# Performance work log

Measured on AMD Instinct MI355X. Metric: run time of the kernel, lower is better.

The kernel has to match this reference:

```python
import jax, jax.numpy as jnp
import numpy as np

B, N, H, E, STEPS = 8, 1024, 128, 4, 3


def setup_inputs() -> dict:
    key = jax.random.key(0)
    ks = jax.random.split(key, 12)
    node_features = jax.random.normal(ks[0], (B, N, H), dtype=jnp.float32)
    edge_matrix = (jax.random.uniform(ks[1], (B, E, N, N)) < 0.01).astype(jnp.float32)
    s = 1.0 / np.sqrt(H)
    We = jax.random.uniform(ks[2], (E, H, H), minval=-s, maxval=s)  # per-edge-type Linear weights (out,in)
    W_ih = jax.random.uniform(ks[3], (3 * H, H), minval=-s, maxval=s)
    W_hh = jax.random.uniform(ks[4], (3 * H, H), minval=-s, maxval=s)
    b_ih = jax.random.uniform(ks[5], (3 * H,), minval=-s, maxval=s)
    b_hh = jax.random.uniform(ks[6], (3 * H,), minval=-s, maxval=s)
    s2 = 1.0 / np.sqrt(2 * H)
    W1 = jax.random.uniform(ks[7], (H, 2 * H), minval=-s2, maxval=s2)
    b1 = jax.random.uniform(ks[8], (H,), minval=-s2, maxval=s2)
    W2 = jax.random.uniform(ks[9], (H, H), minval=-s, maxval=s)
    b2 = jax.random.uniform(ks[10], (H,), minval=-s, maxval=s)
    return dict(node_features=node_features, edge_matrix=edge_matrix, We=We,
                W_ih=W_ih, W_hh=W_hh, b_ih=b_ih, b_hh=b_hh,
                W1=W1, b1=b1, W2=W2, b2=b2)


def _gru_cell(m, h, W_ih, W_hh, b_ih, b_hh):
    # PyTorch GRUCell: gates ordered (r, z, n)
    gi = m @ W_ih.T + b_ih  # (..., 3H)
    gh = h @ W_hh.T + b_hh
    i_r, i_z, i_n = jnp.split(gi, 3, axis=-1)
    h_r, h_z, h_n = jnp.split(gh, 3, axis=-1)
    r = jax.nn.sigmoid(i_r + h_r)
    z = jax.nn.sigmoid(i_z + h_z)
    n = jnp.tanh(i_n + r * h_n)
    return (1.0 - z) * n + z * h


def reference(node_features, edge_matrix, We, W_ih, W_hh, b_ih, b_hh, W1, b1, W2, b2):
    h = node_features  # (B,N,H)
    for _ in range(STEPS):
        # fused per-edge-type Linear: t[b,e,j,k] = sum_h h[b,j,h] * We[e,k,h]
        t = jnp.einsum('bjh,ekh->bejk', h, We)
        # aggregate messages: m[b,i,k] = sum_{e,j} adj[b,e,i,j] * t[b,e,j,k]
        m = jnp.einsum('beij,bejk->bik', edge_matrix, t)
        h = _gru_cell(m, h, W_ih, W_hh, b_ih, b_hh)
    cat = jnp.concatenate([node_features, h], axis=-1)  # (B,N,2H)
    y = jax.nn.relu(cat @ W1.T + b1)
    return y @ W2.T + b2
```

## Files before the change

### kernel.cpp

```cpp
#include <hip/hip_runtime.h>
#include <stdint.h>

typedef short short8 __attribute__((ext_vector_type(8)));
typedef float f32x4 __attribute__((ext_vector_type(4)));

__device__ inline float b2f(unsigned short u) {
    union { float f; uint32_t i; } v; v.i = ((uint32_t)u) << 16; return v.f;
}
__device__ inline unsigned short f2b(float f) {
    union { float f; uint32_t i; } v; v.f = f;
    uint32_t r = v.i + 0x7FFFu + ((v.i >> 16) & 1u);
    return (unsigned short)(r >> 16);
}

#define BB 8
#define NN 1024
#define HH 128
#define EE 4
#define MROWS (BB * NN)
#define NBR_CAP 96
#define CMAX 88
#define RPB 32


__global__ __launch_bounds__(256) void combo(
    const float* __restrict__ adj, unsigned short* __restrict__ cols,
    int* __restrict__ cnt,
    const float* __restrict__ nf, const float* __restrict__ We,
    const float* __restrict__ Wih, const float* __restrict__ Whh,
    const float* __restrict__ bih, const float* __restrict__ bhh,
    const float* __restrict__ W1, const float* __restrict__ W2,
    float* __restrict__ h, unsigned short* __restrict__ hb,
    unsigned short* __restrict__ nfb,
    unsigned short* __restrict__ wcf, unsigned short* __restrict__ wgf,
    unsigned short* __restrict__ w1f, unsigned short* __restrict__ w2f,
    float* __restrict__ bg)
{
    if (blockIdx.x < 8192) {
        int blk = blockIdx.x;
        int gb = blk & 7, q = blk >> 3;
        int row = gb * 4096 + q * 4 + (threadIdx.x >> 6);
        int l = threadIdx.x & 63;
        const float* ar = adj + (size_t)row * NN;
        unsigned short* cr = cols + (size_t)row * NBR_CAP;
        int c = 0;
        for (int it = 0; it < 4; ++it) {
            float4 v = *(const float4*)(ar + it * 256 + l * 4);
            const float* vp = &v.x;
            #pragma unroll
            for (int p = 0; p < 4; ++p) {
                float x = vp[p];
                unsigned long long m = __ballot(x != 0.f);
                if (x != 0.f) {
                    int idx = c + __popcll(m & ((1ull << l) - 1ull));
                    if (idx < CMAX) cr[idx] = (unsigned short)(it * 256 + l * 4 + p);
                }
                c += __popcll(m);
            }
        }
        int bb = row >> 12;
        int cs = c < CMAX ? c : CMAX;
        int pad = (8 - (cs & 7)) & 7;
        if (l < pad) cr[cs + l] = (unsigned short)((8 - bb) << 10);
        if (l == 0) cnt[row] = cs + pad;
        return;
    }
    int blk2 = blockIdx.x - 8192;
    int gb = blk2 & 7, q = blk2 >> 3;
    int tid = (gb * 512 + q) * 256 + threadIdx.x;
    {
        float v = nf[tid];
        h[tid] = v;
        unsigned short b = f2b(v);
        hb[tid] = b;
        nfb[tid] = b;
    }
    if (tid < 128) hb[(size_t)MROWS * 128 + tid] = 0;
    if (tid < 131072) {
        int j = tid & 7, l = (tid >> 3) & 63, f = (tid >> 9) & 31, s = tid >> 14;
        int col = f * 16 + (l & 15);
        int k   = s * 32 + ((l >> 4) << 3) + j;
        int kr = k & 127;
        float v;
        if (col < 256)      v = (k < 128) ? Wih[col * 128 + kr] : Whh[col * 128 + kr];
        else if (col < 384) v = (k < 128) ? Wih[col * 128 + kr] : 0.f;
        else                v = (k < 128) ? 0.f : Whh[(col - 128) * 128 + kr];
        wgf[tid] = f2b(v);
    }
    if (tid < 65536) {
        int j = tid & 7, l = (tid >> 3) & 63, f = (tid >> 9) & 7, s = tid >> 12;
        int col = f * 16 + (l & 15);
        int k   = s * 32 + ((l >> 4) << 3) + j;
        int e = k >> 7, hh2 = k & 127;
        wcf[tid] = f2b(We[(e << 14) + (col << 7) + hh2]);
    }
    if (tid < 32768) {
        int j = tid & 7, l = (tid >> 3) & 63, f = (tid >> 9) & 7, s = tid >> 12;
        int col = f * 16 + (l & 15);
        int k   = s * 32 + ((l >> 4) << 3) + j;
        w1f[tid] = f2b(W1[col * 256 + k]);
    }
    if (tid < 16384) {
        int j = tid & 7, l = (tid >> 3) & 63, f = (tid >> 9) & 7, s = tid >> 12;
        int col = f * 16 + (l & 15);
        int k   = s * 32 + ((l >> 4) << 3) + j;
        w2f[tid] = f2b(W2[col * 128 + k]);
    }
    if (tid < 512) {
        int sec = tid >> 7, k = tid & 127;
        float v;
        if (sec == 0)      v = bih[k] + bhh[k];
        else if (sec == 1) v = bih[128 + k] + bhh[128 + k];
        else if (sec == 2) v = bih[256 + k];
        else               v = bhh[256 + k];
        bg[tid] = v;
    }
}

__global__ __launch_bounds__(256) void aggregate(
    const unsigned short* __restrict__ hb, const unsigned short* __restrict__ cols,
    const int* __restrict__ cnt, unsigned short* __restrict__ ab)
{
    int blk = blockIdx.x;
    int b = blk & 7, i = blk >> 3;
    int e = threadIdx.x >> 6;
    int l2 = (threadIdx.x & 63) * 2;
    int row = ((b << 2) + e) * NN + i;
    int c = cnt[row];
    const unsigned short* cl = cols + (size_t)row * NBR_CAP;
    const unsigned short* hbase = hb + ((size_t)(b << 10)) * HH + l2;
    float a0 = 0.f, a1 = 0.f;
    for (int q = 0; q < c; q += 8) {
        uint4 iv = *(const uint4*)(cl + q);
        uint32_t v0 = *(const uint32_t*)(hbase + (size_t)(iv.x & 0xffffu) * HH);
        uint32_t v1 = *(const uint32_t*)(hbase + (size_t)(iv.x >> 16) * HH);
        uint32_t v2 = *(const uint32_t*)(hbase + (size_t)(iv.y & 0xffffu) * HH);
        uint32_t v3 = *(const uint32_t*)(hbase + (size_t)(iv.y >> 16) * HH);
        uint32_t v4 = *(const uint32_t*)(hbase + (size_t)(iv.z & 0xffffu) * HH);
        uint32_t v5 = *(const uint32_t*)(hbase + (size_t)(iv.z >> 16) * HH);
        uint32_t v6 = *(const uint32_t*)(hbase + (size_t)(iv.w & 0xffffu) * HH);
        uint32_t v7 = *(const uint32_t*)(hbase + (size_t)(iv.w >> 16) * HH);
        a0 += b2f((unsigned short)(v0 & 0xffffu)); a1 += b2f((unsigned short)(v0 >> 16));
        a0 += b2f((unsigned short)(v1 & 0xffffu)); a1 += b2f((unsigned short)(v1 >> 16));
        a0 += b2f((unsigned short)(v2 & 0xffffu)); a1 += b2f((unsigned short)(v2 >> 16));
        a0 += b2f((unsigned short)(v3 & 0xffffu)); a1 += b2f((unsigned short)(v3 >> 16));
        a0 += b2f((unsigned short)(v4 & 0xffffu)); a1 += b2f((unsigned short)(v4 >> 16));
        a0 += b2f((unsigned short)(v5 & 0xffffu)); a1 += b2f((unsigned short)(v5 >> 16));
        a0 += b2f((unsigned short)(v6 & 0xffffu)); a1 += b2f((unsigned short)(v6 >> 16));
        a0 += b2f((unsigned short)(v7 & 0xffffu)); a1 += b2f((unsigned short)(v7 >> 16));
    }
    *(uint32_t*)(ab + ((size_t)((b << 10) + i) * EE + e) * HH + l2) =
        (uint32_t)f2b(a0) | ((uint32_t)f2b(a1) << 16);
}

template<bool LAST>
__global__ __launch_bounds__(512) void step2(
    const unsigned short* __restrict__ ab_g, unsigned short* __restrict__ hb,
    float* __restrict__ h_g,
    const unsigned short* __restrict__ wcf, const unsigned short* __restrict__ wgf,
    const float* __restrict__ bg,
    const unsigned short* __restrict__ nfb,
    const unsigned short* __restrict__ w1f, const float* __restrict__ b1,
    const unsigned short* __restrict__ w2f, const float* __restrict__ b2,
    float* __restrict__ out)
{
    __shared__ unsigned short s_ab[32 * 520];
    __shared__ unsigned short s_m[32 * 136];
    __shared__ unsigned short s_hb[32 * 136];
    __shared__ unsigned short s_nf[32 * 136];
    const int t = threadIdx.x, l = t & 63, wv = t >> 6;
    const int lr = l & 15;
    const int ak = (l >> 4) * 8;
    const int bm = ((blockIdx.x & 7) << 10) + ((blockIdx.x >> 3) * RPB);
    const int kk = wv * 16 + lr;

    float bgr = bg[kk], bgz = bg[128 + kk], bgn = bg[256 + kk], bgh = bg[384 + kk];

    #pragma unroll
    for (int ci = 0; ci < 4; ++ci) {
        int idx = ci * 512 + t;
        int row = idx >> 6, ch = (idx & 63) * 8;
        *(short8*)&s_ab[row * 520 + ch] = *(const short8*)(ab_g + (size_t)(bm + row) * 512 + ch);
    }
    {
        int row = t >> 4, ch = (t & 15) * 8;
        *(short8*)&s_hb[row * 136 + ch] = *(const short8*)(hb + (size_t)(bm + row) * 128 + ch);
        if constexpr (LAST)
            *(short8*)&s_nf[row * 136 + ch] = *(const short8*)(nfb + (size_t)(bm + row) * 128 + ch);
    }
    __syncthreads();

    f32x4 accB[2] = {};
    {
        short8 bf_cur = *(const short8*)(wcf + (((size_t)0 * 8 + wv) * 64 + l) * 8);
        #pragma unroll
        for (int s = 0; s < 16; ++s) {
            short8 bf_next;
            if (s < 15) bf_next = *(const short8*)(wcf + (((size_t)(s + 1) * 8 + wv) * 64 + l) * 8);
            short8 af0 = *(const short8*)&s_ab[lr * 520 + s * 32 + ak];
            short8 af1 = *(const short8*)&s_ab[(16 + lr) * 520 + s * 32 + ak];
            accB[0] = __builtin_amdgcn_mfma_f32_16x16x32_bf16(af0, bf_cur, accB[0], 0, 0, 0);
            accB[1] = __builtin_amdgcn_mfma_f32_16x16x32_bf16(af1, bf_cur, accB[1], 0, 0, 0);
            if (s < 15) bf_cur = bf_next;
        }
    }
    #pragma unroll
    for (int mi = 0; mi < 2; ++mi)
        #pragma unroll
        for (int r = 0; r < 4; ++r)
            s_m[(mi * 16 + (l >> 4) * 4 + r) * 136 + kk] = f2b(accB[mi][r]);
    __syncthreads();

    f32x4 accC[2][4] = {};
    {
        short8 cf[4], nx[4];
        #pragma unroll
        for (int g = 0; g < 4; ++g)
            cf[g] = *(const short8*)(wgf + (((size_t)0 * 32 + g * 8 + wv) * 64 + l) * 8);
        #pragma unroll
        for (int s = 0; s < 8; ++s) {
            if (s < 7) {
                #pragma unroll
                for (int g = 0; g < 4; ++g)
                    nx[g] = *(const short8*)(wgf + (((size_t)(s + 1) * 32 + g * 8 + wv) * 64 + l) * 8);
            }
            short8 af0, af1;
            if (s < 4) {
                af0 = *(const short8*)&s_m[lr * 136 + s * 32 + ak];
                af1 = *(const short8*)&s_m[(16 + lr) * 136 + s * 32 + ak];
            } else {
                af0 = *(const short8*)&s_hb[lr * 136 + (s - 4) * 32 + ak];
                af1 = *(const short8*)&s_hb[(16 + lr) * 136 + (s - 4) * 32 + ak];
            }
            #pragma unroll
            for (int g = 0; g < 4; ++g) {
                accC[0][g] = __builtin_amdgcn_mfma_f32_16x16x32_bf16(af0, cf[g], accC[0][g], 0, 0, 0);
                accC[1][g] = __builtin_amdgcn_mfma_f32_16x16x32_bf16(af1, cf[g], accC[1][g], 0, 0, 0);
            }
            if (s < 7) {
                #pragma unroll
                for (int g = 0; g < 4; ++g) cf[g] = nx[g];
            }
        }
    }

    float hvv[2][4];
    #pragma unroll
    for (int mi = 0; mi < 2; ++mi)
        #pragma unroll
        for (int r = 0; r < 4; ++r) {
            size_t gidx = (size_t)(bm + mi * 16 + (l >> 4) * 4 + r) * 128 + kk;
            float ho = h_g[gidx];
            float rr = 1.f / (1.f + __expf(-(accC[mi][0][r] + bgr)));
            float zz = 1.f / (1.f + __expf(-(accC[mi][1][r] + bgz)));
            float n  = tanhf(accC[mi][2][r] + bgn + rr * (accC[mi][3][r] + bgh));
            float hv = (1.f - zz) * n + zz * ho;
            hvv[mi][r] = hv;
            if constexpr (!LAST) {
                h_g[gidx] = hv;
                hb[gidx]  = f2b(hv);
            }
        }

    if constexpr (LAST) {
        __syncthreads();
        #pragma unroll
        for (int mi = 0; mi < 2; ++mi)
            #pragma unroll
            for (int r = 0; r < 4; ++r)
                s_hb[(mi * 16 + (l >> 4) * 4 + r) * 136 + kk] = f2b(hvv[mi][r]);
        __syncthreads();
        f32x4 accY[2] = {};
        {
            short8 bf_cur = *(const short8*)(w1f + (((size_t)0 * 8 + wv) * 64 + l) * 8);
            #pragma unroll
            for (int s = 0; s < 8; ++s) {
                short8 bf_next;
                if (s < 7) bf_next = *(const short8*)(w1f + (((size_t)(s + 1) * 8 + wv) * 64 + l) * 8);
                short8 af0, af1;
                if (s < 4) {
                    af0 = *(const short8*)&s_nf[lr * 136 + s * 32 + ak];
                    af1 = *(const short8*)&s_nf[(16 + lr) * 136 + s * 32 + ak];
                } else {
                    af0 = *(const short8*)&s_hb[lr * 136 + (s - 4) * 32 + ak];
                    af1 = *(const short8*)&s_hb[(16 + lr) * 136 + (s - 4) * 32 + ak];
                }
                accY[0] = __builtin_amdgcn_mfma_f32_16x16x32_bf16(af0, bf_cur, accY[0], 0, 0, 0);
                accY[1] = __builtin_amdgcn_mfma_f32_16x16x32_bf16(af1, bf_cur, accY[1], 0, 0, 0);
                if (s < 7) bf_cur = bf_next;
            }
        }
        float b1v = b1[kk];
        #pragma unroll
        for (int mi = 0; mi < 2; ++mi)
            #pragma unroll
            for (int r = 0; r < 4; ++r) {
                float v = accY[mi][r] + b1v;
                s_m[(mi * 16 + (l >> 4) * 4 + r) * 136 + kk] = f2b(v > 0.f ? v : 0.f);
            }
        __syncthreads();
        f32x4 accO[2] = {};
        #pragma unroll
        for (int s = 0; s < 4; ++s) {
            short8 af0 = *(const short8*)&s_m[lr * 136 + s * 32 + ak];
            short8 af1 = *(const short8*)&s_m[(16 + lr) * 136 + s * 32 + ak];
            short8 bc = *(const short8*)(w2f + (((size_t)s * 8 + wv) * 64 + l) * 8);
            accO[0] = __builtin_amdgcn_mfma_f32_16x16x32_bf16(af0, bc, accO[0], 0, 0, 0);
            accO[1] = __builtin_amdgcn_mfma_f32_16x16x32_bf16(af1, bc, accO[1], 0, 0, 0);
        }
        float b2v = b2[kk];
        #pragma unroll
        for (int mi = 0; mi < 2; ++mi)
            #pragma unroll
            for (int r = 0; r < 4; ++r)
                out[(size_t)(bm + mi * 16 + (l >> 4) * 4 + r) * 128 + kk] = accO[mi][r] + b2v;
    }
}

extern "C" void kernel_launch(void* const* d_in, const int* in_sizes, int n_in,
                              void* d_out, int out_size, void* d_ws, size_t ws_size,
                              hipStream_t stream) {
    const float* nf  = (const float*)d_in[0];
    const float* adj = (const float*)d_in[1];
    const float* We  = (const float*)d_in[2];
    const float* Wih = (const float*)d_in[3];
    const float* Whh = (const float*)d_in[4];
    const float* bih = (const float*)d_in[5];
    const float* bhh = (const float*)d_in[6];
    const float* W1  = (const float*)d_in[7];
    const float* b1  = (const float*)d_in[8];
    const float* W2  = (const float*)d_in[9];
    const float* b2  = (const float*)d_in[10];
    float* out = (float*)d_out;

    char* p = (char*)d_ws;
    auto take = [&](size_t n) { char* r = p; p += (n + 255) & ~(size_t)255; return r; };
    int* cnt             = (int*)take(32768 * 4);
    unsigned short* cols = (unsigned short*)take((size_t)32768 * NBR_CAP * 2);
    float* h_g           = (float*)take((size_t)MROWS * 128 * 4);
    unsigned short* hb   = (unsigned short*)take((size_t)(MROWS + 1) * 128 * 2);
    unsigned short* nfb  = (unsigned short*)take((size_t)MROWS * 128 * 2);
    unsigned short* ab   = (unsigned short*)take((size_t)MROWS * 512 * 2);
    unsigned short* wcf  = (unsigned short*)take(65536 * 2);
    unsigned short* wgf  = (unsigned short*)take(131072 * 2);
    unsigned short* w1f  = (unsigned short*)take(32768 * 2);
    unsigned short* w2f  = (unsigned short*)take(16384 * 2);
    float* bg            = (float*)take(512 * 4);

    combo<<<12288, 256, 0, stream>>>(adj, cols, cnt, nf, We, Wih, Whh, bih, bhh,
                                     W1, W2, h_g, hb, nfb, wcf, wgf, w1f, w2f, bg);

    aggregate<<<MROWS, 256, 0, stream>>>(hb, cols, cnt, ab);
    step2<false><<<256, 512, 0, stream>>>(ab, hb, h_g, wcf, wgf, bg,
                                          nfb, w1f, b1, w2f, b2, out);
    aggregate<<<MROWS, 256, 0, stream>>>(hb, cols, cnt, ab);
    step2<false><<<256, 512, 0, stream>>>(ab, hb, h_g, wcf, wgf, bg,
                                          nfb, w1f, b1, w2f, b2, out);
    aggregate<<<MROWS, 256, 0, stream>>>(hb, cols, cnt, ab);
    step2<true><<<256, 512, 0, stream>>>(ab, hb, h_g, wcf, wgf, bg,
                                         nfb, w1f, b1, w2f, b2, out);
}
```

Before: 89.84 us.

## Fuse sparse neighbor aggregation into GRU step kernel with ping-pong hidden buffers

Removes the separate aggregate kernel and its bf16 message buffer; each fstep block now gathers neighbor sums for its 32 rows directly into shared memory before the GRU matmuls. The bf16 hidden state is double-buffered (hbA/hbB) so that reads of the old state never race with writes of the new one. Neighbor lists are padded to multiples of 16 and gathered in 16-wide bursts, and the cap drops from 88 to 80. This saves three launches and the ab global round-trip, but only 256 blocks now perform the whole gather, which cuts parallelism, and the lower cap can truncate more neighbor rows.

```diff
diff --git a/kernel.cpp b/kernel.cpp
--- a/kernel.cpp
+++ b/kernel.cpp
@@ -19,9 +19,49 @@
 #define EE 4
 #define MROWS (BB * NN)
 #define NBR_CAP 96
-#define CMAX 88
+#define CMAX 80
 #define RPB 32
 
+
+__device__ __forceinline__ void burst16(
+    const unsigned short* __restrict__ cl, int q,
+    const unsigned short* __restrict__ hbase, float& a0, float& a1)
+{
+    uint4 ia = *(const uint4*)(cl + q);
+    uint4 ib = *(const uint4*)(cl + q + 8);
+    uint32_t v0 = *(const uint32_t*)(hbase + (size_t)(ia.x & 0xffffu) * HH);
+    uint32_t v1 = *(const uint32_t*)(hbase + (size_t)(ia.x >> 16) * HH);
+    uint32_t v2 = *(const uint32_t*)(hbase + (size_t)(ia.y & 0xffffu) * HH);
+    uint32_t v3 = *(const uint32_t*)(hbase + (size_t)(ia.y >> 16) * HH);
+    uint32_t v4 = *(const uint32_t*)(hbase + (size_t)(ia.z & 0xffffu) * HH);
+    uint32_t v5 = *(const uint32_t*)(hbase + (size_t)(ia.z >> 16) * HH);
+    uint32_t v6 = *(const uint32_t*)(hbase + (size_t)(ia.w & 0xffffu) * HH);
+    uint32_t v7 = *(const uint32_t*)(hbase + (size_t)(ia.w >> 16) * HH);
+    uint32_t v8 = *(const uint32_t*)(hbase + (size_t)(ib.x & 0xffffu) * HH);
+    uint32_t v9 = *(const uint32_t*)(hbase + (size_t)(ib.x >> 16) * HH);
+    uint32_t va = *(const uint32_t*)(hbase + (size_t)(ib.y & 0xffffu) * HH);
+    uint32_t vb = *(const uint32_t*)(hbase + (size_t)(ib.y >> 16) * HH);
+    uint32_t vc = *(const uint32_t*)(hbase + (size_t)(ib.z & 0xffffu) * HH);
+    uint32_t vd = *(const uint32_t*)(hbase + (size_t)(ib.z >> 16) * HH);
+    uint32_t ve = *(const uint32_t*)(hbase + (size_t)(ib.w & 0xffffu) * HH);
+    uint32_t vf = *(const uint32_t*)(hbase + (size_t)(ib.w >> 16) * HH);
+    a0 += b2f((unsigned short)(v0 & 0xffffu)); a1 += b2f((unsigned short)(v0 >> 16));
+    a0 += b2f((unsigned short)(v1 & 0xffffu)); a1 += b2f((unsigned short)(v1 >> 16));
+    a0 += b2f((unsigned short)(v2 & 0xffffu)); a1 += b2f((unsigned short)(v2 >> 16));
+    a0 += b2f((unsigned short)(v3 & 0xffffu)); a1 += b2f((unsigned short)(v3 >> 16));
+    a0 += b2f((unsigned short)(v4 & 0xffffu)); a1 += b2f((unsigned short)(v4 >> 16));
+    a0 += b2f((unsigned short)(v5 & 0xffffu)); a1 += b2f((unsigned short)(v5 >> 16));
+    a0 += b2f((unsigned short)(v6 & 0xffffu)); a1 += b2f((unsigned short)(v6 >> 16));
+    a0 += b2f((unsigned short)(v7 & 0xffffu)); a1 += b2f((unsigned short)(v7 >> 16));
+    a0 += b2f((unsigned short)(v8 & 0xffffu)); a1 += b2f((unsigned short)(v8 >> 16));
+    a0 += b2f((unsigned short)(v9 & 0xffffu)); a1 += b2f((unsigned short)(v9 >> 16));
+    a0 += b2f((unsigned short)(va & 0xffffu)); a1 += b2f((unsigned short)(va >> 16));
+    a0 += b2f((unsigned short)(vb & 0xffffu)); a1 += b2f((unsigned short)(vb >> 16));
+    a0 += b2f((unsigned short)(vc & 0xffffu)); a1 += b2f((unsigned short)(vc >> 16));
+    a0 += b2f((unsigned short)(vd & 0xffffu)); a1 += b2f((unsigned short)(vd >> 16));
+    a0 += b2f((unsigned short)(ve & 0xffffu)); a1 += b2f((unsigned short)(ve >> 16));
+    a0 += b2f((unsigned short)(vf & 0xffffu)); a1 += b2f((unsigned short)(vf >> 16));
+}
 
 __global__ __launch_bounds__(256) void combo(
     const float* __restrict__ adj, unsigned short* __restrict__ cols,
@@ -30,8 +70,8 @@
     const float* __restrict__ Wih, const float* __restrict__ Whh,
     const float* __restrict__ bih, const float* __restrict__ bhh,
     const float* __restrict__ W1, const float* __restrict__ W2,
-    float* __restrict__ h, unsigned short* __restrict__ hb,
-    unsigned short* __restrict__ nfb,
+    float* __restrict__ h, unsigned short* __restrict__ hbA,
+    unsigned short* __restrict__ hbB, unsigned short* __restrict__ nfb,
     unsigned short* __restrict__ wcf, unsigned short* __restrict__ wgf,
     unsigned short* __restrict__ w1f, unsigned short* __restrict__ w2f,
     float* __restrict__ bg)
@@ -60,7 +100,8 @@
         }
         int bb = row >> 12;
         int cs = c < CMAX ? c : CMAX;
-        int pad = (8 - (cs & 7)) & 7;
+        int pad = (16 - (cs & 15)) & 15;
+        if (cs == 0) pad = 16;
         if (l < pad) cr[cs + l] = (unsigned short)((8 - bb) << 10);
         if (l == 0) cnt[row] = cs + pad;
         return;
@@ -72,10 +113,13 @@
         float v = nf[tid];
         h[tid] = v;
         unsigned short b = f2b(v);
-        hb[tid] = b;
+        hbA[tid] = b;
         nfb[tid] = b;
     }
-    if (tid < 128) hb[(size_t)MROWS * 128 + tid] = 0;
+    if (tid < 128) {
+        hbA[(size_t)MROWS * 128 + tid] = 0;
+        hbB[(size_t)MROWS * 128 + tid] = 0;
+    }
     if (tid < 131072) {
         int j = tid & 7, l = (tid >> 3) & 63, f = (tid >> 9) & 31, s = tid >> 14;
         int col = f * 16 + (l & 15);
@@ -117,45 +161,10 @@
     }
 }
 
-__global__ __launch_bounds__(256) void aggregate(
-    const unsigned short* __restrict__ hb, const unsigned short* __restrict__ cols,
-    const int* __restrict__ cnt, unsigned short* __restrict__ ab)
-{
-    int blk = blockIdx.x;
-    int b = blk & 7, i = blk >> 3;
-    int e = threadIdx.x >> 6;
-    int l2 = (threadIdx.x & 63) * 2;
-    int row = ((b << 2) + e) * NN + i;
-    int c = cnt[row];
-    const unsigned short* cl = cols + (size_t)row * NBR_CAP;
-    const unsigned short* hbase = hb + ((size_t)(b << 10)) * HH + l2;
-    float a0 = 0.f, a1 = 0.f;
-    for (int q = 0; q < c; q += 8) {
-        uint4 iv = *(const uint4*)(cl + q);
-        uint32_t v0 = *(const uint32_t*)(hbase + (size_t)(iv.x & 0xffffu) * HH);
-        uint32_t v1 = *(const uint32_t*)(hbase + (size_t)(iv.x >> 16) * HH);
-        uint32_t v2 = *(const uint32_t*)(hbase + (size_t)(iv.y & 0xffffu) * HH);
-        uint32_t v3 = *(const uint32_t*)(hbase + (size_t)(iv.y >> 16) * HH);
-        uint32_t v4 = *(const uint32_t*)(hbase + (size_t)(iv.z & 0xffffu) * HH);
-        uint32_t v5 = *(const uint32_t*)(hbase + (size_t)(iv.z >> 16) * HH);
-        uint32_t v6 = *(const uint32_t*)(hbase + (size_t)(iv.w & 0xffffu) * HH);
-        uint32_t v7 = *(const uint32_t*)(hbase + (size_t)(iv.w >> 16) * HH);
-        a0 += b2f((unsigned short)(v0 & 0xffffu)); a1 += b2f((unsigned short)(v0 >> 16));
-        a0 += b2f((unsigned short)(v1 & 0xffffu)); a1 += b2f((unsigned short)(v1 >> 16));
-        a0 += b2f((unsigned short)(v2 & 0xffffu)); a1 += b2f((unsigned short)(v2 >> 16));
-        a0 += b2f((unsigned short)(v3 & 0xffffu)); a1 += b2f((unsigned short)(v3 >> 16));
-        a0 += b2f((unsigned short)(v4 & 0xffffu)); a1 += b2f((unsigned short)(v4 >> 16));
-        a0 += b2f((unsigned short)(v5 & 0xffffu)); a1 += b2f((unsigned short)(v5 >> 16));
-        a0 += b2f((unsigned short)(v6 & 0xffffu)); a1 += b2f((unsigned short)(v6 >> 16));
-        a0 += b2f((unsigned short)(v7 & 0xffffu)); a1 += b2f((unsigned short)(v7 >> 16));
-    }
-    *(uint32_t*)(ab + ((size_t)((b << 10) + i) * EE + e) * HH + l2) =
-        (uint32_t)f2b(a0) | ((uint32_t)f2b(a1) << 16);
-}
-
 template<bool LAST>
-__global__ __launch_bounds__(512) void step2(
-    const unsigned short* __restrict__ ab_g, unsigned short* __restrict__ hb,
+__global__ __launch_bounds__(512, 4) void fstep(
+    const unsigned short* __restrict__ cols, const int* __restrict__ cnt,
+    const unsigned short* __restrict__ hb_in, unsigned short* __restrict__ hb_out,
     float* __restrict__ h_g,
     const unsigned short* __restrict__ wcf, const unsigned short* __restrict__ wgf,
     const float* __restrict__ bg,
@@ -171,22 +180,39 @@
     const int t = threadIdx.x, l = t & 63, wv = t >> 6;
     const int lr = l & 15;
     const int ak = (l >> 4) * 8;
-    const int bm = ((blockIdx.x & 7) << 10) + ((blockIdx.x >> 3) * RPB);
+    const int b = blockIdx.x & 7;
+    const int i0 = (blockIdx.x >> 3) * RPB;
+    const int bm = (b << 10) + i0;
     const int kk = wv * 16 + lr;
-
-    float bgr = bg[kk], bgz = bg[128 + kk], bgn = bg[256 + kk], bgh = bg[384 + kk];
-
-    #pragma unroll
-    for (int ci = 0; ci < 4; ++ci) {
-        int idx = ci * 512 + t;
-        int row = idx >> 6, ch = (idx & 63) * 8;
-        *(short8*)&s_ab[row * 520 + ch] = *(const short8*)(ab_g + (size_t)(bm + row) * 512 + ch);
-    }
+    const int l2 = l * 2;
+
+    const float bgr = bg[kk], bgz = bg[128 + kk], bgn = bg[256 + kk], bgh = bg[384 + kk];
+
     {
         int row = t >> 4, ch = (t & 15) * 8;
-        *(short8*)&s_hb[row * 136 + ch] = *(const short8*)(hb + (size_t)(bm + row) * 128 + ch);
+        *(short8*)&s_hb[row * 136 + ch] = *(const short8*)(hb_in + (size_t)(bm + row) * 128 + ch);
         if constexpr (LAST)
             *(short8*)&s_nf[row * 136 + ch] = *(const short8*)(nfb + (size_t)(bm + row) * 128 + ch);
+    }
+
+    const unsigned short* hbase = hb_in + ((size_t)(b << 10)) * 128 + l2;
+    for (int pp = 0; pp < 16; pp += 2) {
+        int pr0 = wv * 16 + pp, rl0 = pr0 >> 2, e0 = pr0 & 3;
+        int pr1 = pr0 + 1,      rl1 = pr1 >> 2, e1 = pr1 & 3;
+        int ar0 = (((b << 2) + e0) << 10) + i0 + rl0;
+        int ar1 = (((b << 2) + e1) << 10) + i0 + rl1;
+        int c0 = cnt[ar0], c1 = cnt[ar1];
+        const unsigned short* cl0 = cols + (size_t)ar0 * NBR_CAP;
+        const unsigned short* cl1 = cols + (size_t)ar1 * NBR_CAP;
+        float a00 = 0.f, a01 = 0.f, a10 = 0.f, a11 = 0.f;
+        burst16(cl0, 0, hbase, a00, a01);
+        burst16(cl1, 0, hbase, a10, a11);
+        for (int q = 16; q < c0; q += 16) burst16(cl0, q, hbase, a00, a01);
+        for (int q = 16; q < c1; q += 16) burst16(cl1, q, hbase, a10, a11);
+        *(uint32_t*)&s_ab[rl0 * 520 + e0 * 128 + l2] =
+            (uint32_t)f2b(a00) | ((uint32_t)f2b(a01) << 16);
+        *(uint32_t*)&s_ab[rl1 * 520 + e1 * 128 + l2] =
+            (uint32_t)f2b(a10) | ((uint32_t)f2b(a11) << 16);
     }
     __syncthreads();
 
@@ -258,7 +284,7 @@
             hvv[mi][r] = hv;
             if constexpr (!LAST) {
                 h_g[gidx] = hv;
-                hb[gidx]  = f2b(hv);
+                hb_out[gidx] = f2b(hv);
             }
         }
 
@@ -338,9 +364,9 @@
     int* cnt             = (int*)take(32768 * 4);
     unsigned short* cols = (unsigned short*)take((size_t)32768 * NBR_CAP * 2);
     float* h_g           = (float*)take((size_t)MROWS * 128 * 4);
-    unsigned short* hb   = (unsigned short*)take((size_t)(MROWS + 1) * 128 * 2);
+    unsigned short* hbA  = (unsigned short*)take((size_t)(MROWS + 1) * 128 * 2);
+    unsigned short* hbB  = (unsigned short*)take((size_t)(MROWS + 1) * 128 * 2);
     unsigned short* nfb  = (unsigned short*)take((size_t)MROWS * 128 * 2);
-    unsigned short* ab   = (unsigned short*)take((size_t)MROWS * 512 * 2);
     unsigned short* wcf  = (unsigned short*)take(65536 * 2);
     unsigned short* wgf  = (unsigned short*)take(131072 * 2);
     unsigned short* w1f  = (unsigned short*)take(32768 * 2);
@@ -348,15 +374,12 @@
     float* bg            = (float*)take(512 * 4);
 
     combo<<<12288, 256, 0, stream>>>(adj, cols, cnt, nf, We, Wih, Whh, bih, bhh,
-                                     W1, W2, h_g, hb, nfb, wcf, wgf, w1f, w2f, bg);
-
-    aggregate<<<MROWS, 256, 0, stream>>>(hb, cols, cnt, ab);
-    step2<false><<<256, 512, 0, stream>>>(ab, hb, h_g, wcf, wgf, bg,
+                                     W1, W2, h_g, hbA, hbB, nfb, wcf, wgf, w1f, w2f, bg);
+
+    fstep<false><<<256, 512, 0, stream>>>(cols, cnt, hbA, hbB, h_g, wcf, wgf, bg,
                                           nfb, w1f, b1, w2f, b2, out);
-    aggregate<<<MROWS, 256, 0, stream>>>(hb, cols, cnt, ab);
-    step2<false><<<256, 512, 0, stream>>>(ab, hb, h_g, wcf, wgf, bg,
+    fstep<false><<<256, 512, 0, stream>>>(cols, cnt, hbB, hbA, h_g, wcf, wgf, bg,
                                           nfb, w1f, b1, w2f, b2, out);
-    aggregate<<<MROWS, 256, 0, stream>>>(hb, cols, cnt, ab);
-    step2<true><<<256, 512, 0, stream>>>(ab, hb, h_g, wcf, wgf, bg,
+    fstep<true><<<256, 512, 0, stream>>>(cols, cnt, hbA, hbB, h_g, wcf, wgf, bg,
                                          nfb, w1f, b1, w2f, b2, out);
 }
```

Result: faster. 84.67 us (-5.8%).
